# Kernel optimization log

Hardware: AMD Instinct MI355X
Metric: run time of the kernel (lower is better)

The kernel has to match this reference:

```python
import jax, jax.numpy as jnp
import numpy as np

B, T, C, H = 2, 2048, 1024, 16

def setup_inputs() -> dict:
    key = jax.random.key(0)
    ks = jax.random.split(key, 6)
    s = 1.0 / np.sqrt(C)
    return {
        "x": jax.random.normal(ks[0], (B, T, C), jnp.float32),
        "Wq": jax.random.normal(ks[1], (C, C), jnp.float32) * s,
        "Wk": jax.random.normal(ks[2], (C, C), jnp.float32) * s,
        "Wv": jax.random.normal(ks[3], (C, C), jnp.float32) * s,
        "Wp": jax.random.normal(ks[4], (C, C), jnp.float32) * s,
        "bp": jnp.zeros((C,), jnp.float32),
    }

def reference(x, Wq, Wk, Wv, Wp, bp):
    b, t, c = x.shape
    hd = c // H  # head dim
    # Linear layers: torch nn.Linear computes x @ W.T
    def split_heads(y):
        return y.reshape(b, t, H, hd).transpose(0, 2, 1, 3)  # [B,H,T,hd]
    q = split_heads(x @ Wq.T)
    k = split_heads(x @ Wk.T)
    v = split_heads(x @ Wv.T)
    scale = hd ** -0.5
    wei = jnp.einsum('bhqd,bhkd->bhqk', q, k) * scale  # [B,H,T,T]
    causal = jnp.tril(jnp.ones((t, t), bool))
    wei = jnp.where(causal, wei, -jnp.inf)
    wei = jax.nn.softmax(wei, axis=-1)
    out = jnp.einsum('bhqk,bhkd->bhqd', wei, v)  # [B,H,T,hd]
    out = out.transpose(0, 2, 1, 3).reshape(b, t, c)
    return out @ Wp.T + bp
```

## Files before the change

### kernel.cpp

```cpp
#include <hip/hip_runtime.h>
#include <hip/hip_bf16.h>
#include <stdint.h>

#define B_ 2
#define T_ 2048
#define C_ 1024
#define H_ 16
#define HD_ 64
#define NTOK (B_*T_)

typedef __bf16 bf16;
typedef bf16 bf16x4 __attribute__((ext_vector_type(4)));
typedef bf16 bf16x8 __attribute__((ext_vector_type(8)));
typedef float f32x4 __attribute__((ext_vector_type(4)));

static __device__ __forceinline__ f32x4 mfma16(bf16x8 a, bf16x8 b, f32x4 c) {
  return __builtin_amdgcn_mfma_f32_16x16x32_bf16(a, b, c, 0, 0, 0);
}

static __device__ __forceinline__ void gload_lds16(const void* g, void* l) {
  __builtin_amdgcn_global_load_lds(
      (__attribute__((address_space(1))) void*)g,
      (__attribute__((address_space(3))) void*)l, 16, 0, 0);
}

static __device__ __forceinline__ uint32_t cvt_pk_bf16(float lo, float hi) {
  uint32_t r;
  asm("v_cvt_pk_bf16_f32 %0, %1, %2" : "=v"(r) : "v"(lo), "v"(hi));
  return r;
}

__global__ void cvt_all(const float* __restrict__ x,
                        const float* __restrict__ w0, const float* __restrict__ w1,
                        const float* __restrict__ w2, const float* __restrict__ w3,
                        bf16* __restrict__ xb,
                        bf16* __restrict__ d0, bf16* __restrict__ d1,
                        bf16* __restrict__ d2, bf16* __restrict__ d3) {
  const int i = blockIdx.x * 256 + threadIdx.x;
  const int y = blockIdx.y;
  const float* src;
  bf16* dst;
  size_t off4 = 0;
  if (y < 4) {
    src = x; dst = xb; off4 = (size_t)y << 18;
  } else if (y == 4) { src = w0; dst = d0; }
  else if (y == 5)   { src = w1; dst = d1; }
  else if (y == 6)   { src = w2; dst = d2; }
  else               { src = w3; dst = d3; }
  float4 v = reinterpret_cast<const float4*>(src)[off4 + i];
  bf16x4 o;
  o.x = (bf16)v.x; o.y = (bf16)v.y; o.z = (bf16)v.z; o.w = (bf16)v.w;
  reinterpret_cast<bf16x4*>(dst)[off4 + i] = o;
}

__global__ __launch_bounds__(256) void qkv_gemm(
    const bf16* __restrict__ X,
    const bf16* __restrict__ Wq, const bf16* __restrict__ Wk, const bf16* __restrict__ Wv,
    bf16* __restrict__ Q, bf16* __restrict__ K, bf16* __restrict__ VT) {
  __shared__ bf16 As[128 * 64];
  __shared__ bf16 Bs[128 * 64];
  const int z = blockIdx.z;
  const bf16* W = (z == 0) ? Wq : (z == 1) ? Wk : Wv;
  const int n0 = blockIdx.x * 128;
  const int o0 = blockIdx.y * 128;
  const int tid = threadIdx.x;
  const int lane = tid & 63;
  const int w = tid >> 6;
  const int wr = w >> 1, wc = w & 1;
  const int l15 = lane & 15, lhi = lane >> 4;
  const int x7 = l15 & 7;

  f32x4 acc[4][4] = {};

  for (int k0 = 0; k0 < C_; k0 += 64) {
    __syncthreads();
#pragma unroll
    for (int j = 0; j < 4; j++) {
      const int c = tid + j * 256;
      const int row = c >> 3;
      const int scol = ((c & 7) ^ (row & 7)) * 8;
      gload_lds16(X + (size_t)(n0 + row) * C_ + k0 + scol, (char*)As + c * 16);
      gload_lds16(W + (size_t)(o0 + row) * C_ + k0 + scol, (char*)Bs + c * 16);
    }
    __syncthreads();
    bf16x8 a[4][2], b[4][2];
#pragma unroll
    for (int m = 0; m < 4; m++) {
      const int row = wr * 64 + m * 16 + l15;
#pragma unroll
      for (int kk = 0; kk < 2; kk++)
        a[m][kk] = *reinterpret_cast<const bf16x8*>(
            (const char*)As + row * 128 + (((kk * 4 + lhi) ^ x7) * 16));
    }
#pragma unroll
    for (int n = 0; n < 4; n++) {
      const int row = wc * 64 + n * 16 + l15;
#pragma unroll
      for (int kk = 0; kk < 2; kk++)
        b[n][kk] = *reinterpret_cast<const bf16x8*>(
            (const char*)Bs + row * 128 + (((kk * 4 + lhi) ^ x7) * 16));
    }
#pragma unroll
    for (int m = 0; m < 4; m++)
#pragma unroll
      for (int n = 0; n < 4; n++)
#pragma unroll
        for (int kk = 0; kk < 2; kk++)
          acc[m][n] = mfma16(a[m][kk], b[n][kk], acc[m][n]);
  }

  const float QSCALE = 0.125f * 1.44269504f;
#pragma unroll
  for (int m = 0; m < 4; m++) {
#pragma unroll
    for (int n = 0; n < 4; n++) {
#pragma unroll
      for (int r = 0; r < 4; r++) {
        int tok = n0 + wr * 64 + m * 16 + lhi * 4 + r;
        int o = o0 + wc * 64 + n * 16 + l15;
        int bb = tok >> 11, t = tok & (T_ - 1);
        int h = o >> 6, d = o & 63;
        float v = acc[m][n][r];
        if (z == 0) {
          Q[((size_t)(bb * H_ + h) * T_ + t) * HD_ + d] = (bf16)(v * QSCALE);
        } else if (z == 1) {
          K[((size_t)(bb * H_ + h) * T_ + t) * HD_ + d] = (bf16)v;
        } else {
          VT[((size_t)(bb * H_ + h) * HD_ + d) * T_ + t] = (bf16)v;
        }
      }
    }
  }
}

__global__ __launch_bounds__(256, 3) void attn_kernel(
    const bf16* __restrict__ Q, const bf16* __restrict__ K,
    const bf16* __restrict__ VT, bf16* __restrict__ att) {
  __shared__ bf16 Kt[2][64 * 64];
  __shared__ bf16 Vt[2][64 * 64];
  __shared__ bf16 P[4][32][72];
  const int tid = threadIdx.x;
  const int lane = tid & 63;
  const int w = tid >> 6;
  const int l15 = lane & 15, lhi = lane >> 4;
  const int bh = blockIdx.x;
  const int b = bh >> 4, h = bh & 15;
  const int by = (int)blockIdx.y;
  const int qt = (by < 8) ? (15 - by) : (by - 8);
  const int qw0 = qt * 128 + w * 32;
  const bf16* Qb = Q + (size_t)bh * T_ * HD_;
  const bf16* Kb = K + (size_t)bh * T_ * HD_;
  const bf16* Vb = VT + (size_t)bh * HD_ * T_;

  bf16x8 q[2][2];
#pragma unroll
  for (int m = 0; m < 2; m++)
#pragma unroll
    for (int kk = 0; kk < 2; kk++)
      q[m][kk] = *reinterpret_cast<const bf16x8*>(
          &Qb[(size_t)(qw0 + m * 16 + l15) * HD_ + kk * 32 + lhi * 8]);

  f32x4 o_acc[2][4] = {};
  float lsum[2] = {0.f, 0.f};

  const int nt = 2 * qt + 2;

  const int c0 = tid, c1 = tid + 256;
  const int r0 = c0 >> 3, x0 = (c0 & 7) ^ (r0 & 7);
  const int r1 = c1 >> 3, x1 = (c1 & 7) ^ (r1 & 7);

#define STAGE(tt, bb)                                                                \
  do {                                                                               \
    int kv = (tt) * 64;                                                              \
    gload_lds16(Kb + (size_t)(kv + r0) * HD_ + x0 * 8, (char*)&Kt[bb][0] + c0 * 16); \
    gload_lds16(Kb + (size_t)(kv + r1) * HD_ + x1 * 8, (char*)&Kt[bb][0] + c1 * 16); \
    gload_lds16(Vb + (size_t)r0 * T_ + kv + x0 * 8, (char*)&Vt[bb][0] + c0 * 16);    \
    gload_lds16(Vb + (size_t)r1 * T_ + kv + x1 * 8, (char*)&Vt[bb][0] + c1 * 16);    \
  } while (0)

  STAGE(0, 0);
  __syncthreads();
  int cur = 0;

  for (int it = 0; it < nt; ++it) {
    const int kv0 = it * 64;
    if (it + 1 < nt) STAGE(it + 1, cur ^ 1);

    if (kv0 <= qw0 + 31) {
      f32x4 s[2][4] = {};
#pragma unroll
      for (int n = 0; n < 4; n++) {
        const int krow = n * 16 + l15;
#pragma unroll
        for (int kk = 0; kk < 2; kk++) {
          const int kx = (kk * 4 + lhi) ^ (l15 & 7);
          bf16x8 kf = *reinterpret_cast<const bf16x8*>(
              (const char*)&Kt[cur][0] + krow * 128 + kx * 16);
          s[0][n] = mfma16(kf, q[0][kk], s[0][n]);
          s[1][n] = mfma16(kf, q[1][kk], s[1][n]);
        }
      }

      if (kv0 + 63 > qw0) {
#pragma unroll
        for (int m = 0; m < 2; m++) {
          const int qrow = qw0 + m * 16 + l15;
#pragma unroll
          for (int n = 0; n < 4; n++) {
            const int key = kv0 + n * 16 + lhi * 4;
#pragma unroll
            for (int r = 0; r < 4; r++) {
              if (key + r > qrow) s[m][n][r] = -1e30f;
            }
          }
        }
      }
#pragma unroll
      for (int m = 0; m < 2; m++) {
        char* pw = (char*)&P[w][m * 16 + l15][0];
#pragma unroll
        for (int n = 0; n < 4; n++) {
          float p0 = __builtin_amdgcn_exp2f(s[m][n][0]);
          float p1 = __builtin_amdgcn_exp2f(s[m][n][1]);
          float p2 = __builtin_amdgcn_exp2f(s[m][n][2]);
          float p3 = __builtin_amdgcn_exp2f(s[m][n][3]);
          lsum[m] += (p0 + p1) + (p2 + p3);
          uint32_t lo = cvt_pk_bf16(p0, p1);
          uint32_t hi = cvt_pk_bf16(p2, p3);
          *reinterpret_cast<uint2*>(pw + (4 * n + lhi) * 8) = make_uint2(lo, hi);
        }
      }
      bf16x8 pa[2][2];
#pragma unroll
      for (int m = 0; m < 2; m++)
#pragma unroll
        for (int kk = 0; kk < 2; kk++)
          pa[m][kk] = *reinterpret_cast<const bf16x8*>(
              (const char*)&P[w][m * 16 + l15][0] + kk * 64 + lhi * 16);
#pragma unroll
      for (int n = 0; n < 4; n++) {
        const int vrow = n * 16 + l15;
#pragma unroll
        for (int kk = 0; kk < 2; kk++) {
          const int vx = (kk * 4 + lhi) ^ (l15 & 7);
          bf16x8 vf = *reinterpret_cast<const bf16x8*>(
              (const char*)&Vt[cur][0] + vrow * 128 + vx * 16);
          o_acc[0][n] = mfma16(pa[0][kk], vf, o_acc[0][n]);
          o_acc[1][n] = mfma16(pa[1][kk], vf, o_acc[1][n]);
        }
      }
    }
    __syncthreads();
    cur ^= 1;
  }
#undef STAGE

  float lred[2];
#pragma unroll
  for (int m = 0; m < 2; m++) {
    float v = lsum[m];
    v += __shfl_xor(v, 16);
    v += __shfl_xor(v, 32);
    lred[m] = v;
  }
#pragma unroll
  for (int m = 0; m < 2; m++) {
#pragma unroll
    for (int r = 0; r < 4; r++) {
      float rs = __shfl(lred[m], (lane & 48) + lhi * 4 + r);
      float li = 1.f / rs;
      int t = qw0 + m * 16 + lhi * 4 + r;
#pragma unroll
      for (int n = 0; n < 4; n++) {
        int d = n * 16 + l15;
        att[((size_t)(b * T_ + t) * H_ + h) * HD_ + d] = (bf16)(o_acc[m][n][r] * li);
      }
    }
  }
}

__global__ __launch_bounds__(256) void proj_gemm(
    const bf16* __restrict__ A, const bf16* __restrict__ Wp,
    const float* __restrict__ bp, float* __restrict__ out) {
  __shared__ bf16 As[128 * 64];
  __shared__ bf16 Bs[128 * 64];
  const int n0 = blockIdx.x * 128;
  const int o0 = blockIdx.y * 128;
  const int tid = threadIdx.x;
  const int lane = tid & 63;
  const int w = tid >> 6;
  const int wr = w >> 1, wc = w & 1;
  const int l15 = lane & 15, lhi = lane >> 4;
  const int x7 = l15 & 7;

  f32x4 acc[4][4] = {};

  for (int k0 = 0; k0 < C_; k0 += 64) {
    __syncthreads();
#pragma unroll
    for (int j = 0; j < 4; j++) {
      const int c = tid + j * 256;
      const int row = c >> 3;
      const int scol = ((c & 7) ^ (row & 7)) * 8;
      gload_lds16(A + (size_t)(n0 + row) * C_ + k0 + scol, (char*)As + c * 16);
      gload_lds16(Wp + (size_t)(o0 + row) * C_ + k0 + scol, (char*)Bs + c * 16);
    }
    __syncthreads();
    bf16x8 a[4][2], b[4][2];
#pragma unroll
    for (int m = 0; m < 4; m++) {
      const int row = wr * 64 + m * 16 + l15;
#pragma unroll
      for (int kk = 0; kk < 2; kk++)
        a[m][kk] = *reinterpret_cast<const bf16x8*>(
            (const char*)As + row * 128 + (((kk * 4 + lhi) ^ x7) * 16));
    }
#pragma unroll
    for (int n = 0; n < 4; n++) {
      const int row = wc * 64 + n * 16 + l15;
#pragma unroll
      for (int kk = 0; kk < 2; kk++)
        b[n][kk] = *reinterpret_cast<const bf16x8*>(
            (const char*)Bs + row * 128 + (((kk * 4 + lhi) ^ x7) * 16));
    }
#pragma unroll
    for (int m = 0; m < 4; m++)
#pragma unroll
      for (int n = 0; n < 4; n++)
#pragma unroll
        for (int kk = 0; kk < 2; kk++)
          acc[m][n] = mfma16(a[m][kk], b[n][kk], acc[m][n]);
  }

#pragma unroll
  for (int m = 0; m < 4; m++) {
#pragma unroll
    for (int n = 0; n < 4; n++) {
#pragma unroll
      for (int r = 0; r < 4; r++) {
        int tok = n0 + wr * 64 + m * 16 + lhi * 4 + r;
        int o = o0 + wc * 64 + n * 16 + l15;
        out[(size_t)tok * C_ + o] = acc[m][n][r] + bp[o];
      }
    }
  }
}

extern "C" void kernel_launch(void* const* d_in, const int* in_sizes, int n_in,
                              void* d_out, int out_size, void* d_ws, size_t ws_size,
                              hipStream_t stream) {
  const float* x  = (const float*)d_in[0];
  const float* Wq = (const float*)d_in[1];
  const float* Wk = (const float*)d_in[2];
  const float* Wv = (const float*)d_in[3];
  const float* Wp = (const float*)d_in[4];
  const float* bp = (const float*)d_in[5];
  float* out = (float*)d_out;

  char* ws = (char*)d_ws;
  size_t off = 0;
  bf16* xb  = (bf16*)(ws + off); off += (size_t)NTOK * C_ * 2;
  bf16* wqb = (bf16*)(ws + off); off += (size_t)C_ * C_ * 2;
  bf16* wkb = (bf16*)(ws + off); off += (size_t)C_ * C_ * 2;
  bf16* wvb = (bf16*)(ws + off); off += (size_t)C_ * C_ * 2;
  bf16* wpb = (bf16*)(ws + off); off += (size_t)C_ * C_ * 2;
  bf16* Qd  = (bf16*)(ws + off); off += (size_t)NTOK * C_ * 2;
  bf16* Kd  = (bf16*)(ws + off); off += (size_t)NTOK * C_ * 2;
  bf16* VTd = (bf16*)(ws + off); off += (size_t)NTOK * C_ * 2;
  bf16* att = (bf16*)(ws + off); off += (size_t)NTOK * C_ * 2;
  (void)ws_size; (void)out_size; (void)in_sizes; (void)n_in;

  cvt_all<<<dim3(1024, 8), 256, 0, stream>>>(x, Wq, Wk, Wv, Wp, xb, wqb, wkb, wvb, wpb);

  qkv_gemm<<<dim3(NTOK / 128, C_ / 128, 3), 256, 0, stream>>>(xb, wqb, wkb, wvb, Qd, Kd, VTd);
  attn_kernel<<<dim3(B_ * H_, 16), 256, 0, stream>>>(Qd, Kd, VTd, att);
  proj_gemm<<<dim3(NTOK / 128, C_ / 128), 256, 0, stream>>>(att, wpb, bp, out);
}
```

Before: 111.5 us.

## Drop LDS K/V staging in attention; load fragments directly from global per wave

Removes the double-buffered shared-memory staging of K and V tiles and the per-iteration block barrier. Each wave now reads its K and V MFMA fragments straight from global memory (relying on L1/L2) and loops only over its own causal range, so it no longer waits on other waves. The launch-bounds occupancy hint drops from 3 to 2 blocks. The cost is redundant global/cache traffic: all four waves now fetch the same K/V data instead of sharing one LDS copy, and the loads are no longer overlapped with compute.

After: 169.1 us. 1.52x slower.

```diff
diff --git a/kernel.cpp b/kernel.cpp
--- a/kernel.cpp
+++ b/kernel.cpp
@@ -133,11 +133,9 @@
   }
 }
 
-__global__ __launch_bounds__(256, 3) void attn_kernel(
+__global__ __launch_bounds__(256, 2) void attn_kernel(
     const bf16* __restrict__ Q, const bf16* __restrict__ K,
     const bf16* __restrict__ VT, bf16* __restrict__ att) {
-  __shared__ bf16 Kt[2][64 * 64];
-  __shared__ bf16 Vt[2][64 * 64];
   __shared__ bf16 P[4][32][72];
   const int tid = threadIdx.x;
   const int lane = tid & 63;
@@ -163,97 +161,72 @@
   f32x4 o_acc[2][4] = {};
   float lsum[2] = {0.f, 0.f};
 
-  const int nt = 2 * qt + 2;
-
-  const int c0 = tid, c1 = tid + 256;
-  const int r0 = c0 >> 3, x0 = (c0 & 7) ^ (r0 & 7);
-  const int r1 = c1 >> 3, x1 = (c1 & 7) ^ (r1 & 7);
-
-#define STAGE(tt, bb)                                                                \
-  do {                                                                               \
-    int kv = (tt) * 64;                                                              \
-    gload_lds16(Kb + (size_t)(kv + r0) * HD_ + x0 * 8, (char*)&Kt[bb][0] + c0 * 16); \
-    gload_lds16(Kb + (size_t)(kv + r1) * HD_ + x1 * 8, (char*)&Kt[bb][0] + c1 * 16); \
-    gload_lds16(Vb + (size_t)r0 * T_ + kv + x0 * 8, (char*)&Vt[bb][0] + c0 * 16);    \
-    gload_lds16(Vb + (size_t)r1 * T_ + kv + x1 * 8, (char*)&Vt[bb][0] + c1 * 16);    \
-  } while (0)
-
-  STAGE(0, 0);
-  __syncthreads();
-  int cur = 0;
-
-  for (int it = 0; it < nt; ++it) {
+  const int kOff = l15 * HD_ + lhi * 8;
+  const int vOff = l15 * T_ + lhi * 8;
+
+  const int ntw = ((qw0 + 31) >> 6) + 1;
+
+  for (int it = 0; it < ntw; ++it) {
     const int kv0 = it * 64;
-    if (it + 1 < nt) STAGE(it + 1, cur ^ 1);
-
-    if (kv0 <= qw0 + 31) {
-      f32x4 s[2][4] = {};
-#pragma unroll
-      for (int n = 0; n < 4; n++) {
-        const int krow = n * 16 + l15;
-#pragma unroll
-        for (int kk = 0; kk < 2; kk++) {
-          const int kx = (kk * 4 + lhi) ^ (l15 & 7);
-          bf16x8 kf = *reinterpret_cast<const bf16x8*>(
-              (const char*)&Kt[cur][0] + krow * 128 + kx * 16);
-          s[0][n] = mfma16(kf, q[0][kk], s[0][n]);
-          s[1][n] = mfma16(kf, q[1][kk], s[1][n]);
-        }
-      }
-
-      if (kv0 + 63 > qw0) {
-#pragma unroll
-        for (int m = 0; m < 2; m++) {
-          const int qrow = qw0 + m * 16 + l15;
-#pragma unroll
-          for (int n = 0; n < 4; n++) {
-            const int key = kv0 + n * 16 + lhi * 4;
-#pragma unroll
-            for (int r = 0; r < 4; r++) {
-              if (key + r > qrow) s[m][n][r] = -1e30f;
-            }
+    f32x4 s[2][4] = {};
+#pragma unroll
+    for (int n = 0; n < 4; n++) {
+#pragma unroll
+      for (int kk = 0; kk < 2; kk++) {
+        bf16x8 kf = *reinterpret_cast<const bf16x8*>(
+            &Kb[(size_t)(kv0 + n * 16) * HD_ + kOff + kk * 32]);
+        s[0][n] = mfma16(kf, q[0][kk], s[0][n]);
+        s[1][n] = mfma16(kf, q[1][kk], s[1][n]);
+      }
+    }
+
+    if (kv0 + 63 > qw0) {
+#pragma unroll
+      for (int m = 0; m < 2; m++) {
+        const int qrow = qw0 + m * 16 + l15;
+#pragma unroll
+        for (int n = 0; n < 4; n++) {
+          const int key = kv0 + n * 16 + lhi * 4;
+#pragma unroll
+          for (int r = 0; r < 4; r++) {
+            if (key + r > qrow) s[m][n][r] = -1e30f;
           }
         }
       }
-#pragma unroll
-      for (int m = 0; m < 2; m++) {
-        char* pw = (char*)&P[w][m * 16 + l15][0];
-#pragma unroll
-        for (int n = 0; n < 4; n++) {
-          float p0 = __builtin_amdgcn_exp2f(s[m][n][0]);
-          float p1 = __builtin_amdgcn_exp2f(s[m][n][1]);
-          float p2 = __builtin_amdgcn_exp2f(s[m][n][2]);
-          float p3 = __builtin_amdgcn_exp2f(s[m][n][3]);
-          lsum[m] += (p0 + p1) + (p2 + p3);
-          uint32_t lo = cvt_pk_bf16(p0, p1);
-          uint32_t hi = cvt_pk_bf16(p2, p3);
-          *reinterpret_cast<uint2*>(pw + (4 * n + lhi) * 8) = make_uint2(lo, hi);
-        }
-      }
-      bf16x8 pa[2][2];
-#pragma unroll
-      for (int m = 0; m < 2; m++)
-#pragma unroll
-        for (int kk = 0; kk < 2; kk++)
-          pa[m][kk] = *reinterpret_cast<const bf16x8*>(
-              (const char*)&P[w][m * 16 + l15][0] + kk * 64 + lhi * 16);
+    }
+#pragma unroll
+    for (int m = 0; m < 2; m++) {
+      char* pw = (char*)&P[w][m * 16 + l15][0];
 #pragma unroll
       for (int n = 0; n < 4; n++) {
-        const int vrow = n * 16 + l15;
-#pragma unroll
-        for (int kk = 0; kk < 2; kk++) {
-          const int vx = (kk * 4 + lhi) ^ (l15 & 7);
-          bf16x8 vf = *reinterpret_cast<const bf16x8*>(
-              (const char*)&Vt[cur][0] + vrow * 128 + vx * 16);
-          o_acc[0][n] = mfma16(pa[0][kk], vf, o_acc[0][n]);
-          o_acc[1][n] = mfma16(pa[1][kk], vf, o_acc[1][n]);
-        }
-      }
-    }
-    __syncthreads();
-    cur ^= 1;
-  }
-#undef STAGE
+        float p0 = __builtin_amdgcn_exp2f(s[m][n][0]);
+        float p1 = __builtin_amdgcn_exp2f(s[m][n][1]);
+        float p2 = __builtin_amdgcn_exp2f(s[m][n][2]);
+        float p3 = __builtin_amdgcn_exp2f(s[m][n][3]);
+        lsum[m] += (p0 + p1) + (p2 + p3);
+        uint32_t lo = cvt_pk_bf16(p0, p1);
+        uint32_t hi = cvt_pk_bf16(p2, p3);
+        *reinterpret_cast<uint2*>(pw + (4 * n + lhi) * 8) = make_uint2(lo, hi);
+      }
+    }
+    bf16x8 pa[2][2];
+#pragma unroll
+    for (int m = 0; m < 2; m++)
+#pragma unroll
+      for (int kk = 0; kk < 2; kk++)
+        pa[m][kk] = *reinterpret_cast<const bf16x8*>(
+            (const char*)&P[w][m * 16 + l15][0] + kk * 64 + lhi * 16);
+#pragma unroll
+    for (int n = 0; n < 4; n++) {
+#pragma unroll
+      for (int kk = 0; kk < 2; kk++) {
+        bf16x8 vf = *reinterpret_cast<const bf16x8*>(
+            &Vb[(size_t)(n * 16) * T_ + vOff + kv0 + kk * 32]);
+        o_acc[0][n] = mfma16(pa[0][kk], vf, o_acc[0][n]);
+        o_acc[1][n] = mfma16(pa[1][kk], vf, o_acc[1][n]);
+      }
+    }
+  }
 
   float lred[2];
 #pragma unroll
```

## Split attention KV range across two wave groups per block and reduce in LDS

Applied to the files above, without the earlier changes.

The attention kernel now launches 512 threads per block. Two groups of four waves each cover one half of the causal KV tiles for the same query rows, and each group has its own double-buffered K/V shared-memory buffers. The upper group writes its partial O accumulators and row sums to an LDS reduction buffer, and the lower group adds them and writes the normalized output. This halves the serial KV loop per block and targets the latency of the long causal tiles, at the cost of more LDS per block, possibly lower occupancy, and an extra reduction step.

Measured after the change: 107.5 us, median of 3. 3.6% less time.

```diff
diff --git a/kernel.cpp b/kernel.cpp
--- a/kernel.cpp
+++ b/kernel.cpp
@@ -133,15 +133,18 @@
   }
 }
 
-__global__ __launch_bounds__(256, 3) void attn_kernel(
+__global__ __launch_bounds__(512) void attn_kernel(
     const bf16* __restrict__ Q, const bf16* __restrict__ K,
     const bf16* __restrict__ VT, bf16* __restrict__ att) {
-  __shared__ bf16 Kt[2][64 * 64];
-  __shared__ bf16 Vt[2][64 * 64];
-  __shared__ bf16 P[4][32][72];
+  __shared__ bf16 KtL[2][64 * 64], VtL[2][64 * 64];
+  __shared__ bf16 KtH[2][64 * 64], VtH[2][64 * 64];
+  __shared__ bf16 P[8][32][72];
+  __shared__ float Red[4][64][35];
   const int tid = threadIdx.x;
   const int lane = tid & 63;
-  const int w = tid >> 6;
+  const int wid = tid >> 6;
+  const int w = wid & 3;
+  const int hig = wid >> 2;
   const int l15 = lane & 15, lhi = lane >> 4;
   const int bh = blockIdx.x;
   const int b = bh >> 4, h = bh & 15;
@@ -152,6 +155,9 @@
   const bf16* Kb = K + (size_t)bh * T_ * HD_;
   const bf16* Vb = VT + (size_t)bh * HD_ * T_;
 
+  bf16 (*Kt)[64 * 64] = hig ? KtH : KtL;
+  bf16 (*Vt)[64 * 64] = hig ? VtH : VtL;
+
   bf16x8 q[2][2];
 #pragma unroll
   for (int m = 0; m < 2; m++)
@@ -163,9 +169,13 @@
   f32x4 o_acc[2][4] = {};
   float lsum[2] = {0.f, 0.f};
 
-  const int nt = 2 * qt + 2;
-
-  const int c0 = tid, c1 = tid + 256;
+  const int nIter = qt + 1;
+  const int tBeg = hig ? (qt + 1) : 0;
+  const int ntw = ((qw0 + 31) >> 6) + 1;
+  const int tEnd = hig ? ntw : (qt + 1);
+
+  const int t256 = tid & 255;
+  const int c0 = t256, c1 = t256 + 256;
   const int r0 = c0 >> 3, x0 = (c0 & 7) ^ (r0 & 7);
   const int r1 = c1 >> 3, x1 = (c1 & 7) ^ (r1 & 7);
 
@@ -178,15 +188,15 @@
     gload_lds16(Vb + (size_t)r1 * T_ + kv + x1 * 8, (char*)&Vt[bb][0] + c1 * 16);    \
   } while (0)
 
-  STAGE(0, 0);
+  STAGE(tBeg, 0);
   __syncthreads();
-  int cur = 0;
-
-  for (int it = 0; it < nt; ++it) {
-    const int kv0 = it * 64;
-    if (it + 1 < nt) STAGE(it + 1, cur ^ 1);
-
-    if (kv0 <= qw0 + 31) {
+
+  for (int i = 0; i < nIter; ++i) {
+    const int cur = i & 1;
+    if (i + 1 < nIter) STAGE(tBeg + i + 1, cur ^ 1);
+    const int tile = tBeg + i;
+    if (tile < tEnd) {
+      const int kv0 = tile * 64;
       f32x4 s[2][4] = {};
 #pragma unroll
       for (int n = 0; n < 4; n++) {
@@ -217,7 +227,7 @@
       }
 #pragma unroll
       for (int m = 0; m < 2; m++) {
-        char* pw = (char*)&P[w][m * 16 + l15][0];
+        char* pw = (char*)&P[wid][m * 16 + l15][0];
 #pragma unroll
         for (int n = 0; n < 4; n++) {
           float p0 = __builtin_amdgcn_exp2f(s[m][n][0]);
@@ -236,7 +246,7 @@
 #pragma unroll
         for (int kk = 0; kk < 2; kk++)
           pa[m][kk] = *reinterpret_cast<const bf16x8*>(
-              (const char*)&P[w][m * 16 + l15][0] + kk * 64 + lhi * 16);
+              (const char*)&P[wid][m * 16 + l15][0] + kk * 64 + lhi * 16);
 #pragma unroll
       for (int n = 0; n < 4; n++) {
         const int vrow = n * 16 + l15;
@@ -251,29 +261,53 @@
       }
     }
     __syncthreads();
-    cur ^= 1;
   }
 #undef STAGE
 
-  float lred[2];
-#pragma unroll
-  for (int m = 0; m < 2; m++) {
-    float v = lsum[m];
-    v += __shfl_xor(v, 16);
-    v += __shfl_xor(v, 32);
-    lred[m] = v;
-  }
-#pragma unroll
-  for (int m = 0; m < 2; m++) {
-#pragma unroll
-    for (int r = 0; r < 4; r++) {
-      float rs = __shfl(lred[m], (lane & 48) + lhi * 4 + r);
-      float li = 1.f / rs;
-      int t = qw0 + m * 16 + lhi * 4 + r;
-#pragma unroll
-      for (int n = 0; n < 4; n++) {
-        int d = n * 16 + l15;
-        att[((size_t)(b * T_ + t) * H_ + h) * HD_ + d] = (bf16)(o_acc[m][n][r] * li);
+  if (hig) {
+    float* rd = &Red[w][lane][0];
+#pragma unroll
+    for (int m = 0; m < 2; m++)
+#pragma unroll
+      for (int n = 0; n < 4; n++)
+#pragma unroll
+        for (int r = 0; r < 4; r++)
+          rd[(m * 4 + n) * 4 + r] = o_acc[m][n][r];
+    rd[32] = lsum[0];
+    rd[33] = lsum[1];
+  }
+  __syncthreads();
+  if (!hig) {
+    const float* rd = &Red[w][lane][0];
+#pragma unroll
+    for (int m = 0; m < 2; m++) {
+#pragma unroll
+      for (int n = 0; n < 4; n++)
+#pragma unroll
+        for (int r = 0; r < 4; r++)
+          o_acc[m][n][r] += rd[(m * 4 + n) * 4 + r];
+      lsum[m] += rd[32 + m];
+    }
+    float lred[2];
+#pragma unroll
+    for (int m = 0; m < 2; m++) {
+      float v = lsum[m];
+      v += __shfl_xor(v, 16);
+      v += __shfl_xor(v, 32);
+      lred[m] = v;
+    }
+#pragma unroll
+    for (int m = 0; m < 2; m++) {
+#pragma unroll
+      for (int r = 0; r < 4; r++) {
+        float rs = __shfl(lred[m], (lane & 48) + lhi * 4 + r);
+        float li = 1.f / rs;
+        int t = qw0 + m * 16 + lhi * 4 + r;
+#pragma unroll
+        for (int n = 0; n < 4; n++) {
+          int d = n * 16 + l15;
+          att[((size_t)(b * T_ + t) * H_ + h) * HD_ + d] = (bf16)(o_acc[m][n][r] * li);
+        }
       }
     }
   }
@@ -373,6 +407,6 @@
   cvt_all<<<dim3(1024, 8), 256, 0, stream>>>(x, Wq, Wk, Wv, Wp, xb, wqb, wkb, wvb, wpb);
 
   qkv_gemm<<<dim3(NTOK / 128, C_ / 128, 3), 256, 0, stream>>>(xb, wqb, wkb, wvb, Qd, Kd, VTd);
-  attn_kernel<<<dim3(B_ * H_, 16), 256, 0, stream>>>(Qd, Kd, VTd, att);
+  attn_kernel<<<dim3(B_ * H_, 16), 512, 0, stream>>>(Qd, Kd, VTd, att);
   proj_gemm<<<dim3(NTOK / 128, C_ / 128), 256, 0, stream>>>(att, wpb, bp, out);
 }
```
